# Performance work log

Hardware: AMD Instinct MI355X
Metric: run time of the kernel (lower is better)

## Reference

```python
import jax, jax.numpy as jnp
import numpy as np

EMBED = 1024
HEADS = 16
HEAD_DIM = EMBED // HEADS


def setup_inputs() -> dict:
    key = jax.random.key(0)
    ks = jax.random.split(key, 6)
    N, S, E = 2, 2048, EMBED
    value = jax.random.normal(ks[0], (N, S, E), dtype=jnp.float32)
    k = jax.random.normal(ks[1], (N, S, E), dtype=jnp.float32)
    q = jax.random.normal(ks[2], (N, S, E), dtype=jnp.float32)
    mask = jax.random.randint(ks[3], (N, 1, S, S), 0, 2, dtype=jnp.int32)
    W_fc = jax.random.normal(ks[4], (E, E), dtype=jnp.float32) * (1.0 / np.sqrt(E))
    b_fc = jax.random.normal(ks[5], (E,), dtype=jnp.float32) * 0.01
    return {"value": value, "key": k, "query": q, "mask": mask, "W_fc": W_fc, "b_fc": b_fc}


def reference(value, key, query, mask, W_fc, b_fc):
    N, Sq, E = query.shape
    Sk = key.shape[1]
    Sv = value.shape[1]
    # NOTE: the original module never applies its q/k/v Linear layers (source bug);
    # it only reshapes into heads.
    v = value.reshape(N, Sv, HEADS, HEAD_DIM)
    k = key.reshape(N, Sk, HEADS, HEAD_DIM)
    q = query.reshape(N, Sq, HEADS, HEAD_DIM)
    # energy: [N, H, Q, K]
    energy = jnp.einsum('nqhd,nkhd->nhqk', q, k)
    energy = jnp.where(mask == 0, jnp.float32(-1e20), energy)
    # scale by sqrt(embed_size) as in the source (not sqrt(head_dim))
    attention = jax.nn.softmax(energy / jnp.sqrt(jnp.float32(E)), axis=3)
    out = jnp.einsum('nhql,nlhd->nqhd', attention, v).reshape(N, Sq, E)
    # torch Linear: x @ W.T + b
    out = out @ W_fc.T + b_fc
    return out
```

## Files before the change

kernel.cpp:

```cpp
#include <hip/hip_runtime.h>
#include <hip/hip_bf16.h>
#include <math.h>

#define S_LEN 2048
#define EMB   1024
#define HEADS 16
#define HDIM  64
#define SPLIT 4

#define C_SCALE   0.045084439f
#define BIAS_OK  -2.0f
#define BIAS_MASK -1.0e9f

#define NE  ((size_t)2 * S_LEN * EMB)
#define NL  ((size_t)2 * S_LEN * HEADS)
#define NMB ((size_t)2 * S_LEN * S_LEN / 64)

typedef __bf16 bf16x8 __attribute__((ext_vector_type(8)));
typedef float  f32x4  __attribute__((ext_vector_type(4)));

__device__ __forceinline__ bf16x8 cvt8(const float* v) {
    bf16x8 r;
#pragma unroll
    for (int i = 0; i < 8; ++i) r[i] = (__bf16)v[i];
    return r;
}
__device__ __forceinline__ unsigned long long pack4(float a, float b, float c, float d) {
    __bf16 t[4] = {(__bf16)a, (__bf16)b, (__bf16)c, (__bf16)d};
    return *(unsigned long long*)t;
}
__device__ __forceinline__ void gld_lds16(const void* g, void* l) {
    __builtin_amdgcn_global_load_lds(
        (const __attribute__((address_space(1))) void*)g,
        (__attribute__((address_space(3))) void*)l, 16, 0, 0);
}

__global__ __launch_bounds__(256)
void prepass_kernel(const float* __restrict__ Kp, const float* __restrict__ Vp,
                    const float* __restrict__ Qp, const float* __restrict__ Wf,
                    const int* __restrict__ Mp,
                    __bf16* __restrict__ Kb, __bf16* __restrict__ Vb,
                    __bf16* __restrict__ Qb, __bf16* __restrict__ Wb,
                    unsigned long long* __restrict__ Mb) {
    const int bid = blockIdx.x, tid = threadIdx.x;
    if (bid < 6144) {
        const float* s; __bf16* d;
        if (bid < 2048)      { s = Kp; d = Kb; }
        else if (bid < 4096) { s = Vp; d = Vb; }
        else                 { s = Qp; d = Qb; }
        size_t i = (((size_t)(bid & 2047)) * 256 + tid) * 8;
        float t[8];
        *(float4*)&t[0] = *(const float4*)(s + i);
        *(float4*)&t[4] = *(const float4*)(s + i + 4);
        *(bf16x8*)(d + i) = cvt8(t);
    } else if (bid < 6656) {
        size_t i = (((size_t)(bid - 6144)) * 256 + tid) * 8;
        float t[8];
        *(float4*)&t[0] = *(const float4*)(Wf + i);
        *(float4*)&t[4] = *(const float4*)(Wf + i + 4);
        *(bf16x8*)(Wb + i) = cvt8(t);
    } else {
        const int w = tid >> 6, lane = tid & 63;
        const int wave = (bid - 6656) * 4 + w;
#pragma unroll 4
        for (int it = 0; it < 16; ++it) {
            size_t chunk = (size_t)wave * 16 + it;
            int4 v = *(const int4*)(Mp + chunk * 256 + lane * 4);
            unsigned long long b0 = __ballot(v.x != 0);
            unsigned long long b1 = __ballot(v.y != 0);
            unsigned long long b2 = __ballot(v.z != 0);
            unsigned long long b3 = __ballot(v.w != 0);
            if (lane < 4) {
                int sh = lane * 16;
                unsigned long long wv = ((b0 >> sh) & 0xFFFFULL)
                                      | (((b1 >> sh) & 0xFFFFULL) << 16)
                                      | (((b2 >> sh) & 0xFFFFULL) << 32)
                                      | (((b3 >> sh) & 0xFFFFULL) << 48);
                Mb[chunk * 4 + lane] = wv;
            }
        }
    }
}

__global__ __launch_bounds__(256)
void attn_kernel(const __bf16* __restrict__ Vb, const __bf16* __restrict__ Kb,
                 const __bf16* __restrict__ Qb, const unsigned long long* __restrict__ Mb,
                 __bf16* __restrict__ Opart, float* __restrict__ Lpart) {
    __shared__ __bf16 Klds[64 * 64];
    __shared__ __bf16 Vtlds[64 * 64];
    __shared__ __bf16 Plds[4][16 * 64];

    const int tid  = threadIdx.x;
    const int lane = tid & 63;
    const int w    = tid >> 6;
    const int nblk = 2 * HEADS * SPLIT * 16;
    const int bid  = (blockIdx.x & 7) * (nblk / 8) + (blockIdx.x >> 3);
    const int qt = bid & 15;
    const int sp = (bid >> 4) & (SPLIT - 1);
    const int h  = (bid >> 6) & 15;
    const int n  = bid >> 10;

    const int ql = lane & 15;
    const int g  = lane >> 4;

    const __bf16* qbase = Qb + (size_t)n * S_LEN * EMB + h * HDIM;
    const __bf16* kbase = Kb + (size_t)n * S_LEN * EMB + h * HDIM;
    const __bf16* vbase = Vb + (size_t)n * S_LEN * EMB + h * HDIM;

    const int qw = qt * 128 + w * 32;

    bf16x8 qfrag[2][2];
#pragma unroll
    for (int qf = 0; qf < 2; ++qf) {
        const __bf16* qp = qbase + (size_t)(qw + qf * 16 + ql) * EMB + g * 8;
#pragma unroll
        for (int ks = 0; ks < 2; ++ks)
            qfrag[qf][ks] = *(const bf16x8*)(qp + ks * 32);
    }

    f32x4 oacc[2][4] = {};
    f32x4 lacc[2] = {};
    bf16x8 aon;
#pragma unroll
    for (int i = 0; i < 8; ++i) aon[i] = (__bf16)1.0f;

    const int sk  = tid >> 2;
    const int sdq = (tid & 3) * 16;
    const int d0  = (tid & 31) * 2;
    const int kv8 = (tid >> 5) * 8;

    const int kvbase = sp * (S_LEN / SPLIT);
    const int niter  = (S_LEN / SPLIT) / 64;

#pragma unroll 1
    for (int t = 0; t < niter; ++t) {
        const int kv0 = kvbase + t * 64;
        __syncthreads();
        {
            const __bf16* kp = kbase + (size_t)(kv0 + sk) * EMB + sdq;
            bf16x8 ka = *(const bf16x8*)kp;
            bf16x8 kc = *(const bf16x8*)(kp + 8);
            *(bf16x8*)((char*)Klds + sk * 128 + ((sdq * 2)       ^ ((sk & 7) << 4))) = ka;
            *(bf16x8*)((char*)Klds + sk * 128 + (((sdq + 8) * 2) ^ ((sk & 7) << 4))) = kc;

            const __bf16* vp = vbase + (size_t)(kv0 + kv8) * EMB + d0;
            unsigned short r0[8], r1[8];
#pragma unroll
            for (int j = 0; j < 8; ++j) {
                ushort2 tv = *(const ushort2*)(vp + (size_t)j * EMB);
                r0[j] = tv.x; r1[j] = tv.y;
            }
            *(bf16x8*)((char*)Vtlds + d0 * 128       + ((kv8 * 2) ^ ((d0 & 7) << 4)))       = *(bf16x8*)r0;
            *(bf16x8*)((char*)Vtlds + (d0 + 1) * 128 + ((kv8 * 2) ^ (((d0 + 1) & 7) << 4))) = *(bf16x8*)r1;
        }
        __syncthreads();

        f32x4 e[4][2];
        __builtin_amdgcn_s_setprio(1);
#pragma unroll
        for (int jt = 0; jt < 4; ++jt) {
            int row = jt * 16 + ql;
            bf16x8 k0 = *(const bf16x8*)((char*)Klds + row * 128 + ((g * 16)      ^ ((row & 7) << 4)));
            bf16x8 k1 = *(const bf16x8*)((char*)Klds + row * 128 + ((64 + g * 16) ^ ((row & 7) << 4)));
#pragma unroll
            for (int qf = 0; qf < 2; ++qf) {
                f32x4 z = {};
                z         = __builtin_amdgcn_mfma_f32_16x16x32_bf16(k0, qfrag[qf][0], z, 0, 0, 0);
                e[jt][qf] = __builtin_amdgcn_mfma_f32_16x16x32_bf16(k1, qfrag[qf][1], z, 0, 0, 0);
            }
        }
        __builtin_amdgcn_s_setprio(0);

        bf16x8 pf[2][2];
#pragma unroll
        for (int qf = 0; qf < 2; ++qf) {
            const unsigned long long m64 =
                Mb[((size_t)(n * S_LEN + qw + qf * 16 + ql) << 5) + (kv0 >> 6)];
#pragma unroll
            for (int jt = 0; jt < 4; ++jt) {
                unsigned long long tsh = m64 >> (jt * 4 + g);
                unsigned lo = (unsigned)tsh, hi = (unsigned)(tsh >> 32);
                float p0 = exp2f(fmaf(e[jt][qf][0], C_SCALE, (lo & 1u)         ? BIAS_OK : BIAS_MASK));
                float p1 = exp2f(fmaf(e[jt][qf][1], C_SCALE, ((lo >> 16) & 1u) ? BIAS_OK : BIAS_MASK));
                float p2 = exp2f(fmaf(e[jt][qf][2], C_SCALE, (hi & 1u)         ? BIAS_OK : BIAS_MASK));
                float p3 = exp2f(fmaf(e[jt][qf][3], C_SCALE, ((hi >> 16) & 1u) ? BIAS_OK : BIAS_MASK));
                *(unsigned long long*)((char*)Plds[w] + ql * 128 +
                    ((jt * 32 + g * 8) ^ ((ql & 7) << 4))) = pack4(p0, p1, p2, p3);
            }
#pragma unroll
            for (int ks = 0; ks < 2; ++ks)
                pf[ks][qf] = *(const bf16x8*)((char*)Plds[w] + ql * 128 +
                    ((ks * 64 + g * 16) ^ ((ql & 7) << 4)));
            lacc[qf] = __builtin_amdgcn_mfma_f32_16x16x32_bf16(aon, pf[0][qf], lacc[qf], 0, 0, 0);
            lacc[qf] = __builtin_amdgcn_mfma_f32_16x16x32_bf16(aon, pf[1][qf], lacc[qf], 0, 0, 0);
        }

        __builtin_amdgcn_s_setprio(1);
#pragma unroll
        for (int dt = 0; dt < 4; ++dt) {
            int row = dt * 16 + ql;
            bf16x8 v0 = *(const bf16x8*)((char*)Vtlds + row * 128 + ((g * 16)      ^ ((row & 7) << 4)));
            bf16x8 v1 = *(const bf16x8*)((char*)Vtlds + row * 128 + ((64 + g * 16) ^ ((row & 7) << 4)));
#pragma unroll
            for (int qf = 0; qf < 2; ++qf) {
                oacc[qf][dt] = __builtin_amdgcn_mfma_f32_16x16x32_bf16(v0, pf[0][qf], oacc[qf][dt], 0, 0, 0);
                oacc[qf][dt] = __builtin_amdgcn_mfma_f32_16x16x32_bf16(v1, pf[1][qf], oacc[qf][dt], 0, 0, 0);
            }
        }
        __builtin_amdgcn_s_setprio(0);
    }

#pragma unroll
    for (int qf = 0; qf < 2; ++qf) {
        const int q = qw + qf * 16 + ql;
        __bf16* op = Opart + (size_t)sp * NE + ((size_t)n * S_LEN + q) * EMB + h * HDIM;
#pragma unroll
        for (int dt = 0; dt < 4; ++dt)
            *(unsigned long long*)(op + dt * 16 + g * 4) =
                pack4(oacc[qf][dt][0], oacc[qf][dt][1], oacc[qf][dt][2], oacc[qf][dt][3]);
        if (g == 0)
            Lpart[(size_t)sp * NL + ((size_t)n * S_LEN + q) * HEADS + h] = lacc[qf][0];
    }
}

__global__ __launch_bounds__(256)
void reduce_kernel(const __bf16* __restrict__ Opart, const float* __restrict__ Lpart,
                   __bf16* __restrict__ X) {
    size_t e0 = ((size_t)blockIdx.x * 256 + threadIdx.x) * 8;
    size_t hr = e0 >> 6;
    float l = 0.f;
#pragma unroll
    for (int s = 0; s < SPLIT; ++s) l += Lpart[s * NL + hr];
    float inv = 1.f / l;
    float acc[8] = {};
#pragma unroll
    for (int s = 0; s < SPLIT; ++s) {
        bf16x8 v = *(const bf16x8*)(Opart + s * NE + e0);
#pragma unroll
        for (int i = 0; i < 8; ++i) acc[i] += (float)v[i];
    }
    bf16x8 r;
#pragma unroll
    for (int i = 0; i < 8; ++i) r[i] = (__bf16)(acc[i] * inv);
    *(bf16x8*)(X + e0) = r;
}

__global__ __launch_bounds__(256)
void fc_kernel(const __bf16* __restrict__ X, const __bf16* __restrict__ Wb,
               const float* __restrict__ bfc, float* __restrict__ Out) {
    __shared__ __bf16 Al[128 * 32];
    __shared__ __bf16 Bl[128 * 32];
    const int tid = threadIdx.x, lane = tid & 63, w = tid >> 6;
    const int ql = lane & 15, g = lane >> 4;
    const int bm = blockIdx.x >> 3, bn = blockIdx.x & 7;
    const int wr = w >> 1, wc = w & 1;

    const int rowL = lane >> 2;
    const int colE = (lane & 3) * 8;

    f32x4 acc[4][4] = {};

    for (int k0 = 0; k0 < EMB; k0 += 32) {
        __syncthreads();
        const int q0 = w * 2, q1 = w * 2 + 1;
        gld_lds16(X  + (size_t)(bm * 128 + q0 * 16 + rowL) * EMB + k0 + colE, Al + q0 * 512);
        gld_lds16(X  + (size_t)(bm * 128 + q1 * 16 + rowL) * EMB + k0 + colE, Al + q1 * 512);
        gld_lds16(Wb + (size_t)(bn * 128 + q0 * 16 + rowL) * EMB + k0 + colE, Bl + q0 * 512);
        gld_lds16(Wb + (size_t)(bn * 128 + q1 * 16 + rowL) * EMB + k0 + colE, Bl + q1 * 512);
        __syncthreads();

        bf16x8 a[4], b[4];
#pragma unroll
        for (int mi = 0; mi < 4; ++mi)
            a[mi] = *(const bf16x8*)(Al + (wr * 64 + mi * 16 + ql) * 32 + g * 8);
#pragma unroll
        for (int nj = 0; nj < 4; ++nj)
            b[nj] = *(const bf16x8*)(Bl + (wc * 64 + nj * 16 + ql) * 32 + g * 8);
#pragma unroll
        for (int mi = 0; mi < 4; ++mi)
#pragma unroll
            for (int nj = 0; nj < 4; ++nj)
                acc[mi][nj] = __builtin_amdgcn_mfma_f32_16x16x32_bf16(a[mi], b[nj], acc[mi][nj], 0, 0, 0);
    }

#pragma unroll
    for (int nj = 0; nj < 4; ++nj) {
        int col = bn * 128 + wc * 64 + nj * 16 + ql;
        float bias = bfc[col];
#pragma unroll
        for (int mi = 0; mi < 4; ++mi) {
            int row0 = bm * 128 + wr * 64 + mi * 16 + g * 4;
#pragma unroll
            for (int r = 0; r < 4; ++r)
                Out[(size_t)(row0 + r) * EMB + col] = acc[mi][nj][r] + bias;
        }
    }
}

extern "C" void kernel_launch(void* const* d_in, const int* in_sizes, int n_in,
                              void* d_out, int out_size, void* d_ws, size_t ws_size,
                              hipStream_t stream) {
    const float* Vp = (const float*)d_in[0];
    const float* Kp = (const float*)d_in[1];
    const float* Qp = (const float*)d_in[2];
    const int*   Mp = (const int*)d_in[3];
    const float* Wf = (const float*)d_in[4];
    const float* bf = (const float*)d_in[5];
    float* Out = (float*)d_out;

    char* p = (char*)d_ws;
    __bf16* Opart = (__bf16*)p;             p += SPLIT * NE * 2;
    float*  Lpart = (float*)p;              p += SPLIT * NL * 4;
    __bf16* Kb    = (__bf16*)p;             p += NE * 2;
    __bf16* Vb    = (__bf16*)p;             p += NE * 2;
    __bf16* Qb    = (__bf16*)p;             p += NE * 2;
    __bf16* Wb    = (__bf16*)p;             p += (size_t)EMB * EMB * 2;
    unsigned long long* Mb = (unsigned long long*)p;

    prepass_kernel<<<dim3(7168), dim3(256), 0, stream>>>(Kp, Vp, Qp, Wf, Mp, Kb, Vb, Qb, Wb, Mb);
    attn_kernel<<<dim3(2 * HEADS * SPLIT * 16), dim3(256), 0, stream>>>(Vb, Kb, Qb, Mb, Opart, Lpart);
    reduce_kernel<<<dim3(NE / 8 / 256), dim3(256), 0, stream>>>(Opart, Lpart, Opart);
    fc_kernel<<<dim3((2 * S_LEN / 128) * (EMB / 128)), dim3(256), 0, stream>>>(Opart, Wb, bf, Out);
}
```

Measured before the change: 136.2 us.

## Fuse fp32-to-bf16 conversion of Q/K/V into attention tile loads

Drops the prepass conversion of Q, K and V to bf16 workspace buffers. The attention kernel now reads the fp32 inputs directly and converts them while staging K/V tiles into LDS, which removes a full read-write pass over three large tensors. The trade-off is that each attention block reads twice as many bytes per K/V tile, and those tiles are re-read by every q-tile and split block. Separately, masking now multiplies the exponential by a 0/1 mask bit instead of selecting a large negative bias, and it uses the hardware exp2 builtin.

```diff
diff --git a/kernel.cpp b/kernel.cpp
--- a/kernel.cpp
+++ b/kernel.cpp
@@ -10,7 +10,6 @@
 
 #define C_SCALE   0.045084439f
 #define BIAS_OK  -2.0f
-#define BIAS_MASK -1.0e9f
 
 #define NE  ((size_t)2 * S_LEN * EMB)
 #define NL  ((size_t)2 * S_LEN * HEADS)
@@ -36,32 +35,18 @@
 }
 
 __global__ __launch_bounds__(256)
-void prepass_kernel(const float* __restrict__ Kp, const float* __restrict__ Vp,
-                    const float* __restrict__ Qp, const float* __restrict__ Wf,
-                    const int* __restrict__ Mp,
-                    __bf16* __restrict__ Kb, __bf16* __restrict__ Vb,
-                    __bf16* __restrict__ Qb, __bf16* __restrict__ Wb,
-                    unsigned long long* __restrict__ Mb) {
+void prepass_kernel(const float* __restrict__ Wf, const int* __restrict__ Mp,
+                    __bf16* __restrict__ Wb, unsigned long long* __restrict__ Mb) {
     const int bid = blockIdx.x, tid = threadIdx.x;
-    if (bid < 6144) {
-        const float* s; __bf16* d;
-        if (bid < 2048)      { s = Kp; d = Kb; }
-        else if (bid < 4096) { s = Vp; d = Vb; }
-        else                 { s = Qp; d = Qb; }
-        size_t i = (((size_t)(bid & 2047)) * 256 + tid) * 8;
-        float t[8];
-        *(float4*)&t[0] = *(const float4*)(s + i);
-        *(float4*)&t[4] = *(const float4*)(s + i + 4);
-        *(bf16x8*)(d + i) = cvt8(t);
-    } else if (bid < 6656) {
-        size_t i = (((size_t)(bid - 6144)) * 256 + tid) * 8;
+    if (bid < 512) {
+        size_t i = ((size_t)bid * 256 + tid) * 8;
         float t[8];
         *(float4*)&t[0] = *(const float4*)(Wf + i);
         *(float4*)&t[4] = *(const float4*)(Wf + i + 4);
         *(bf16x8*)(Wb + i) = cvt8(t);
     } else {
         const int w = tid >> 6, lane = tid & 63;
-        const int wave = (bid - 6656) * 4 + w;
+        const int wave = (bid - 512) * 4 + w;
 #pragma unroll 4
         for (int it = 0; it < 16; ++it) {
             size_t chunk = (size_t)wave * 16 + it;
@@ -83,8 +68,8 @@
 }
 
 __global__ __launch_bounds__(256)
-void attn_kernel(const __bf16* __restrict__ Vb, const __bf16* __restrict__ Kb,
-                 const __bf16* __restrict__ Qb, const unsigned long long* __restrict__ Mb,
+void attn_kernel(const float* __restrict__ Vp, const float* __restrict__ Kp,
+                 const float* __restrict__ Qp, const unsigned long long* __restrict__ Mb,
                  __bf16* __restrict__ Opart, float* __restrict__ Lpart) {
     __shared__ __bf16 Klds[64 * 64];
     __shared__ __bf16 Vtlds[64 * 64];
@@ -103,19 +88,23 @@
     const int ql = lane & 15;
     const int g  = lane >> 4;
 
-    const __bf16* qbase = Qb + (size_t)n * S_LEN * EMB + h * HDIM;
-    const __bf16* kbase = Kb + (size_t)n * S_LEN * EMB + h * HDIM;
-    const __bf16* vbase = Vb + (size_t)n * S_LEN * EMB + h * HDIM;
+    const float* qbase = Qp + (size_t)n * S_LEN * EMB + h * HDIM;
+    const float* kbase = Kp + (size_t)n * S_LEN * EMB + h * HDIM;
+    const float* vbase = Vp + (size_t)n * S_LEN * EMB + h * HDIM;
 
     const int qw = qt * 128 + w * 32;
 
     bf16x8 qfrag[2][2];
 #pragma unroll
     for (int qf = 0; qf < 2; ++qf) {
-        const __bf16* qp = qbase + (size_t)(qw + qf * 16 + ql) * EMB + g * 8;
-#pragma unroll
-        for (int ks = 0; ks < 2; ++ks)
-            qfrag[qf][ks] = *(const bf16x8*)(qp + ks * 32);
+        const float* qp = qbase + (size_t)(qw + qf * 16 + ql) * EMB + g * 8;
+#pragma unroll
+        for (int ks = 0; ks < 2; ++ks) {
+            float tmp[8];
+            *(float4*)&tmp[0] = *(const float4*)(qp + ks * 32);
+            *(float4*)&tmp[4] = *(const float4*)(qp + ks * 32 + 4);
+            qfrag[qf][ks] = cvt8(tmp);
+        }
     }
 
     f32x4 oacc[2][4] = {};
@@ -123,6 +112,9 @@
     bf16x8 aon;
 #pragma unroll
     for (int i = 0; i < 8; ++i) aon[i] = (__bf16)1.0f;
+
+    const unsigned long long* mb0 = Mb + ((size_t)(n * S_LEN + qw + ql) << 5);
+    const unsigned long long* mb1 = Mb + ((size_t)(n * S_LEN + qw + 16 + ql) << 5);
 
     const int sk  = tid >> 2;
     const int sdq = (tid & 3) * 16;
@@ -137,21 +129,24 @@
         const int kv0 = kvbase + t * 64;
         __syncthreads();
         {
-            const __bf16* kp = kbase + (size_t)(kv0 + sk) * EMB + sdq;
-            bf16x8 ka = *(const bf16x8*)kp;
-            bf16x8 kc = *(const bf16x8*)(kp + 8);
-            *(bf16x8*)((char*)Klds + sk * 128 + ((sdq * 2)       ^ ((sk & 7) << 4))) = ka;
-            *(bf16x8*)((char*)Klds + sk * 128 + (((sdq + 8) * 2) ^ ((sk & 7) << 4))) = kc;
-
-            const __bf16* vp = vbase + (size_t)(kv0 + kv8) * EMB + d0;
-            unsigned short r0[8], r1[8];
+            const float* kp = kbase + (size_t)(kv0 + sk) * EMB + sdq;
+            float tk[16];
+            *(float4*)&tk[0]  = *(const float4*)kp;
+            *(float4*)&tk[4]  = *(const float4*)(kp + 4);
+            *(float4*)&tk[8]  = *(const float4*)(kp + 8);
+            *(float4*)&tk[12] = *(const float4*)(kp + 12);
+            *(bf16x8*)((char*)Klds + sk * 128 + ((sdq * 2)       ^ ((sk & 7) << 4))) = cvt8(&tk[0]);
+            *(bf16x8*)((char*)Klds + sk * 128 + (((sdq + 8) * 2) ^ ((sk & 7) << 4))) = cvt8(&tk[8]);
+
+            const float* vp = vbase + (size_t)(kv0 + kv8) * EMB + d0;
+            float r0[8], r1[8];
 #pragma unroll
             for (int j = 0; j < 8; ++j) {
-                ushort2 tv = *(const ushort2*)(vp + (size_t)j * EMB);
+                float2 tv = *(const float2*)(vp + (size_t)j * EMB);
                 r0[j] = tv.x; r1[j] = tv.y;
             }
-            *(bf16x8*)((char*)Vtlds + d0 * 128       + ((kv8 * 2) ^ ((d0 & 7) << 4)))       = *(bf16x8*)r0;
-            *(bf16x8*)((char*)Vtlds + (d0 + 1) * 128 + ((kv8 * 2) ^ (((d0 + 1) & 7) << 4))) = *(bf16x8*)r1;
+            *(bf16x8*)((char*)Vtlds + d0 * 128       + ((kv8 * 2) ^ ((d0 & 7) << 4)))       = cvt8(r0);
+            *(bf16x8*)((char*)Vtlds + (d0 + 1) * 128 + ((kv8 * 2) ^ (((d0 + 1) & 7) << 4))) = cvt8(r1);
         }
         __syncthreads();
 
@@ -174,16 +169,19 @@
         bf16x8 pf[2][2];
 #pragma unroll
         for (int qf = 0; qf < 2; ++qf) {
-            const unsigned long long m64 =
-                Mb[((size_t)(n * S_LEN + qw + qf * 16 + ql) << 5) + (kv0 >> 6)];
+            const unsigned long long m64 = (qf ? mb1 : mb0)[(kv0 >> 6)];
+            const unsigned u  = (unsigned)(m64 >> g);
+            const unsigned uh = (unsigned)(m64 >> (g + 32));
 #pragma unroll
             for (int jt = 0; jt < 4; ++jt) {
-                unsigned long long tsh = m64 >> (jt * 4 + g);
-                unsigned lo = (unsigned)tsh, hi = (unsigned)(tsh >> 32);
-                float p0 = exp2f(fmaf(e[jt][qf][0], C_SCALE, (lo & 1u)         ? BIAS_OK : BIAS_MASK));
-                float p1 = exp2f(fmaf(e[jt][qf][1], C_SCALE, ((lo >> 16) & 1u) ? BIAS_OK : BIAS_MASK));
-                float p2 = exp2f(fmaf(e[jt][qf][2], C_SCALE, (hi & 1u)         ? BIAS_OK : BIAS_MASK));
-                float p3 = exp2f(fmaf(e[jt][qf][3], C_SCALE, ((hi >> 16) & 1u) ? BIAS_OK : BIAS_MASK));
+                float mb_0 = (float)((u  >> (jt * 4))      & 1u);
+                float mb_1 = (float)((u  >> (jt * 4 + 16)) & 1u);
+                float mb_2 = (float)((uh >> (jt * 4))      & 1u);
+                float mb_3 = (float)((uh >> (jt * 4 + 16)) & 1u);
+                float p0 = __builtin_amdgcn_exp2f(fmaf(e[jt][qf][0], C_SCALE, BIAS_OK)) * mb_0;
+                float p1 = __builtin_amdgcn_exp2f(fmaf(e[jt][qf][1], C_SCALE, BIAS_OK)) * mb_1;
+                float p2 = __builtin_amdgcn_exp2f(fmaf(e[jt][qf][2], C_SCALE, BIAS_OK)) * mb_2;
+                float p3 = __builtin_amdgcn_exp2f(fmaf(e[jt][qf][3], C_SCALE, BIAS_OK)) * mb_3;
                 *(unsigned long long*)((char*)Plds[w] + ql * 128 +
                     ((jt * 32 + g * 8) ^ ((ql & 7) << 4))) = pack4(p0, p1, p2, p3);
             }
@@ -311,14 +309,11 @@
     char* p = (char*)d_ws;
     __bf16* Opart = (__bf16*)p;             p += SPLIT * NE * 2;
     float*  Lpart = (float*)p;              p += SPLIT * NL * 4;
-    __bf16* Kb    = (__bf16*)p;             p += NE * 2;
-    __bf16* Vb    = (__bf16*)p;             p += NE * 2;
-    __bf16* Qb    = (__bf16*)p;             p += NE * 2;
     __bf16* Wb    = (__bf16*)p;             p += (size_t)EMB * EMB * 2;
     unsigned long long* Mb = (unsigned long long*)p;
 
-    prepass_kernel<<<dim3(7168), dim3(256), 0, stream>>>(Kp, Vp, Qp, Wf, Mp, Kb, Vb, Qb, Wb, Mb);
-    attn_kernel<<<dim3(2 * HEADS * SPLIT * 16), dim3(256), 0, stream>>>(Vb, Kb, Qb, Mb, Opart, Lpart);
+    prepass_kernel<<<dim3(1024), dim3(256), 0, stream>>>(Wf, Mp, Wb, Mb);
+    attn_kernel<<<dim3(2 * HEADS * SPLIT * 16), dim3(256), 0, stream>>>(Vp, Kp, Qp, Mb, Opart, Lpart);
     reduce_kernel<<<dim3(NE / 8 / 256), dim3(256), 0, stream>>>(Opart, Lpart, Opart);
     fc_kernel<<<dim3((2 * S_LEN / 128) * (EMB / 128)), dim3(256), 0, stream>>>(Opart, Wb, bf, Out);
 }
```

Measured after the change: 128.3 us. -5.8%, faster.
